# Performance work log

Hardware: AMD Instinct MI355X
Metric: run time of the kernel (lower is better)

## Reference

```python
import jax, jax.numpy as jnp
import numpy as np

SLOPE = 0.2

def setup_inputs() -> dict:
    key = jax.random.key(0)
    ks = jax.random.split(key, 24)
    B, O, M, Nb = 16, 1024, 64, 64
    in_ope, in_mas, in_arc, out = 16, 8, 8, 32
    f = lambda k, s: jax.random.normal(k, s, dtype=jnp.float32)
    adj = lambda k, s: jax.random.randint(k, s, 0, 2).astype(jnp.float32)
    return {
        'adj0': adj(ks[0], (O, M)),
        'adj1': adj(ks[1], (O, M)),
        'adj2': adj(ks[2], (O, Nb)),
        'adj3': adj(ks[3], (O, Nb)),
        'batch_idxes': jnp.arange(B, dtype=jnp.int64),
        'feat_opes': f(ks[4], (B, O, in_ope)),
        'feat_mas': f(ks[5], (B, M, in_mas)),
        'feat_buf': f(ks[6], (B, Nb, in_mas)),
        'feat_arc_ma_in': f(ks[7], (B, O, M, in_arc)),
        'feat_arc_buf_in': f(ks[8], (B, O, Nb, in_arc)),
        'feat_arc_ma_out': f(ks[9], (B, O, M, in_arc)),
        'feat_arc_buf_out': f(ks[10], (B, O, Nb, in_arc)),
        'W_ope': f(ks[11], (in_ope, out)) * 0.2,
        'W_mas': f(ks[12], (in_mas, out)) * 0.2,
        'W_buf': f(ks[13], (in_mas, out)) * 0.2,
        'W_arc_in': f(ks[14], (in_arc, out)) * 0.2,
        'W_arc_out': f(ks[15], (in_arc, out)) * 0.2,
        'attn_ope': jax.random.uniform(ks[16], (out,), dtype=jnp.float32),
        'attn_mas': jax.random.uniform(ks[17], (out,), dtype=jnp.float32),
        'attn_arc': jax.random.uniform(ks[18], (out,), dtype=jnp.float32),
    }

def _branch(adj_in, adj_out, p_ope, p_node, p_arc_in, p_arc_out, e_ope, e_node, e_arc_in, e_arc_out):
    # adj_*: [O,N]; e_ope: [B,O,1]; e_node: [B,N,1]; e_arc_*: [B,O,N,1]
    def scores(A2, e_arc):
        A = A2[None, :, :, None]                               # [1,O,N,1]
        a = A * e_ope[:, :, None, :] + e_arc + A * e_node[:, None, :, :]
        return jax.nn.leaky_relu(a, SLOPE)                     # [B,O,N,1]
    eik_in = scores(adj_in, e_arc_in)
    eik_out = scores(adj_out, e_arc_out)
    ekk = jax.nn.leaky_relu(e_node + e_node, SLOPE)            # [B,N,1]
    def alphas(A2, eik):
        e = jnp.concatenate([eik, ekk[:, None]], axis=1)       # [B,O+1,N,1]
        mask = jnp.concatenate([A2 == 1.0, jnp.ones((1, A2.shape[1]), dtype=bool)], axis=0)
        e = jnp.where(mask[None, :, :, None], e, -jnp.inf)
        return jax.nn.softmax(e[..., 0], axis=1)               # [B,O+1,N] over neighbors
    al_in = alphas(adj_in, eik_in)
    al_out = alphas(adj_out, eik_out)
    # NOTE: Wmu_out replicates the original's missing-parens expression exactly
    Wmu_in = jnp.sum((p_arc_in + p_ope[:, :, None, :]) * al_in[:, :-1, :, None], axis=1)   # [B,N,F]
    Wmu_out = jnp.sum(p_arc_out + p_ope[:, :, None, :] * al_out[:, :-1, :, None], axis=1)  # [B,N,F]
    Wmu_kk = p_node * (al_in[:, -1, :] + al_out[:, -1, :])[..., None]                      # [B,N,F]
    return jax.nn.sigmoid(Wmu_in + Wmu_out + Wmu_kk)

def reference(adj0, adj1, adj2, adj3, batch_idxes, feat_opes, feat_mas, feat_buf,
              feat_arc_ma_in, feat_arc_buf_in, feat_arc_ma_out, feat_arc_buf_out,
              W_ope, W_mas, W_buf, W_arc_in, W_arc_out, attn_ope, attn_mas, attn_arc):
    p_ope = feat_opes @ W_ope              # [B,O,F]
    p_mas = feat_mas @ W_mas               # [B,M,F]
    p_buf = feat_buf @ W_buf               # [B,Nb,F]
    p_arc_ma_in = feat_arc_ma_in @ W_arc_in
    p_arc_buf_in = feat_arc_buf_in @ W_arc_in
    p_arc_ma_out = feat_arc_ma_out @ W_arc_out
    p_arc_buf_out = feat_arc_buf_out @ W_arc_out
    score = lambda p, a: jnp.sum(p * a, axis=-1, keepdims=True)
    e_ope = score(p_ope, attn_ope)
    e_mas = score(p_mas, attn_mas)
    e_buf = score(p_buf, attn_mas)         # original uses attn_mas for buffers too
    nu_mas = _branch(adj0, adj1, p_ope, p_mas, p_arc_ma_in, p_arc_ma_out,
                     e_ope, e_mas, score(p_arc_ma_in, attn_arc), score(p_arc_ma_out, attn_arc))
    nu_buf = _branch(adj2, adj3, p_ope, p_buf, p_arc_buf_in, p_arc_buf_out,
                     e_ope, e_buf, score(p_arc_buf_in, attn_arc), score(p_arc_buf_out, attn_arc))
    return (nu_mas, nu_buf)
```

## Files before the change

### kernel.cpp

```cpp
#include <hip/hip_runtime.h>
#include <math.h>

#define B_   16
#define O_   1024
#define M_   64
#define C_   32
#define INO  16
#define INA  8
#define SLOPE 0.2f

#define NF    50
#define NCOL  (2*B_*M_)

#define WS_EOPE   0
#define WS_ENODE  (WS_EOPE + B_*O_)
#define WS_PNODE  (WS_ENODE + 2*B_*M_)
#define WS_WARC   (WS_PNODE + 2*B_*M_*C_)
#define WS_ACC    (WS_WARC + 16)

__device__ inline float rfl(float x) {
    return __int_as_float(__builtin_amdgcn_readfirstlane(__float_as_int(x)));
}

__global__ void k_pre(const float* __restrict__ feat_opes,
                      const float* __restrict__ feat_mas,
                      const float* __restrict__ feat_buf,
                      const float* __restrict__ W_ope,
                      const float* __restrict__ W_mas,
                      const float* __restrict__ W_buf,
                      const float* __restrict__ W_arc_in,
                      const float* __restrict__ W_arc_out,
                      const float* __restrict__ attn_ope,
                      const float* __restrict__ attn_mas,
                      const float* __restrict__ attn_arc,
                      float* __restrict__ ws) {
    int tid = threadIdx.x;
    int bid = blockIdx.x;
    if (bid < 64) {
        __shared__ float wo[INO];
        if (tid < INO) {
            float s = 0.f;
            for (int c = 0; c < C_; ++c) s += W_ope[tid*C_ + c]*attn_ope[c];
            wo[tid] = s;
        }
        __syncthreads();
        int idx = bid*256 + tid;
        const float* f = feat_opes + idx*INO;
        float s = 0.f;
#pragma unroll
        for (int j = 0; j < INO; ++j) s += f[j]*wo[j];
        ws[WS_EOPE + idx] = s;
    } else if (bid < 72) {
        int idx = (bid - 64)*256 + tid;
        int br  = idx >> 10;
        int rem = idx & 1023;
        const float* f = (br == 0 ? feat_mas : feat_buf) + rem*INA;
        const float* W = (br == 0 ? W_mas : W_buf);
        float f8[INA];
#pragma unroll
        for (int k = 0; k < INA; ++k) f8[k] = f[k];
        float e = 0.f;
        float* pn = ws + WS_PNODE + idx*C_;
        for (int c = 0; c < C_; ++c) {
            float s = 0.f;
#pragma unroll
            for (int k = 0; k < INA; ++k) s += f8[k]*W[k*C_ + c];
            pn[c] = s;
            e += s*attn_mas[c];
        }
        ws[WS_ENODE + idx] = e;
    } else if (bid == 72) {
        if (tid < 16) {
            const float* W = (tid < 8) ? W_arc_in : W_arc_out;
            int k = tid & 7;
            float s = 0.f;
            for (int c = 0; c < C_; ++c) s += W[k*C_ + c]*attn_arc[c];
            ws[WS_WARC + tid] = s;
        }
    } else {
        int idx = (bid - 73)*256 + tid;
        ws[WS_ACC + idx] = 0.f;
    }
}

__global__ __launch_bounds__(256) void k_main(
        const float* __restrict__ adj0, const float* __restrict__ adj1,
        const float* __restrict__ adj2, const float* __restrict__ adj3,
        const float* __restrict__ feat_opes,
        const float* __restrict__ fin_ma,  const float* __restrict__ fin_buf,
        const float* __restrict__ fout_ma, const float* __restrict__ fout_buf,
        float* __restrict__ ws) {
    int tid = threadIdx.x;
    int l  = tid & 63;
    int y  = __builtin_amdgcn_readfirstlane(tid >> 6);
    int oh = y & 1;
    int mh = y >> 1;
    int h  = l & 1;
    int m  = mh*32 + (l >> 1);
    int bid = blockIdx.x;
    int chunk = bid & 31;
    int t = bid >> 5;
    int b  = t & (B_ - 1);
    int br = t >> 4;
    int o0 = chunk*32 + oh*16;

    const float* A_in  = br ? adj2 : adj0;
    const float* A_out = br ? adj3 : adj1;
    const float* fin   = br ? fin_buf  : fin_ma;
    const float* fout  = br ? fout_buf : fout_ma;

    float4 wsi = *(const float4*)(ws + WS_WARC + h*4);
    float4 wso = *(const float4*)(ws + WS_WARC + 8 + h*4);

    float e_node_m = ws[WS_ENODE + (br*B_ + b)*M_ + m];

    const float* eop = ws + WS_EOPE + b*O_ + o0;
    float eo[16];
#pragma unroll
    for (int i = 0; i < 16; ++i) eo[i] = rfl(eop[i]);

    const float* Ai = A_in  + o0*M_ + m;
    const float* Ao = A_out + o0*M_ + m;
    unsigned amA = 0, amB = 0;
#pragma unroll
    for (int i = 0; i < 16; ++i) {
        amA |= (Ai[i*M_] == 1.0f) ? (1u << i) : 0u;
        amB |= (Ao[i*M_] == 1.0f) ? (1u << i) : 0u;
    }

    const float* Pi = fin  + ((size_t)(b*O_ + o0)*M_ + m)*INA + h*4;
    const float* Po = fout + ((size_t)(b*O_ + o0)*M_ + m)*INA + h*4;
    const float* fo = feat_opes + (size_t)(b*O_ + o0)*INO + h*8;
    const int OSTR = M_*INA;

    float l_in = 0.f, l_out = 0.f;
    float ai4[4], so4[4], aoi8[8], aoo8[8];
#pragma unroll
    for (int k = 0; k < 4; ++k) { ai4[k] = 0.f; so4[k] = 0.f; }
#pragma unroll
    for (int j = 0; j < 8; ++j) { aoi8[j] = 0.f; aoo8[j] = 0.f; }

#pragma unroll
    for (int it = 0; it < 16; ++it) {
        float4 xi = *(const float4*)(Pi + (size_t)it*OSTR);
        float4 xo = *(const float4*)(Po + (size_t)it*OSTR);
        float4 f0 = *(const float4*)(fo + it*INO);
        float4 f1 = *(const float4*)(fo + it*INO + 4);
        float pi_ = xi.x*wsi.x + xi.y*wsi.y + xi.z*wsi.z + xi.w*wsi.w;
        float po_ = xo.x*wso.x + xo.y*wso.y + xo.z*wso.z + xo.w*wso.w;
        float din = pi_ + __shfl_xor(pi_, 1, 64);
        float dot = po_ + __shfl_xor(po_, 1, 64);
        float base = eo[it] + e_node_m;
        float si = base + din;  si = si > 0.f ? si : SLOPE*si;
        float so = base + dot;  so = so > 0.f ? so : SLOPE*so;
        float wi  = (amA & (1u << it)) ? __expf(si) : 0.f;
        float wo_ = (amB & (1u << it)) ? __expf(so) : 0.f;
        l_in += wi; l_out += wo_;
        ai4[0] += wi*xi.x; ai4[1] += wi*xi.y; ai4[2] += wi*xi.z; ai4[3] += wi*xi.w;
        so4[0] += xo.x;    so4[1] += xo.y;    so4[2] += xo.z;    so4[3] += xo.w;
        aoi8[0] += wi*f0.x;  aoi8[1] += wi*f0.y;  aoi8[2] += wi*f0.z;  aoi8[3] += wi*f0.w;
        aoi8[4] += wi*f1.x;  aoi8[5] += wi*f1.y;  aoi8[6] += wi*f1.z;  aoi8[7] += wi*f1.w;
        aoo8[0] += wo_*f0.x; aoo8[1] += wo_*f0.y; aoo8[2] += wo_*f0.z; aoo8[3] += wo_*f0.w;
        aoo8[4] += wo_*f1.x; aoo8[5] += wo_*f1.y; aoo8[6] += wo_*f1.z; aoo8[7] += wo_*f1.w;
    }

    __shared__ float red[2][NF][64];
    if (h == 0) {
        red[oh][0][m]  = l_in;
        red[oh][25][m] = l_out;
#pragma unroll
        for (int k = 0; k < 4; ++k) { red[oh][1+k][m]  = ai4[k]; red[oh][42+k][m] = so4[k]; }
#pragma unroll
        for (int j = 0; j < 8; ++j) { red[oh][9+j][m]  = aoi8[j]; red[oh][26+j][m] = aoo8[j]; }
    } else {
#pragma unroll
        for (int k = 0; k < 4; ++k) { red[oh][5+k][m]  = ai4[k]; red[oh][46+k][m] = so4[k]; }
#pragma unroll
        for (int j = 0; j < 8; ++j) { red[oh][17+j][m] = aoi8[j]; red[oh][34+j][m] = aoo8[j]; }
    }
    __syncthreads();

    float* acc = ws + WS_ACC;
    int colbase = (br*B_ + b)*M_;
    for (int i = tid; i < NF*64; i += 256) {
        int f  = i >> 6;
        int m2 = i & 63;
        unsafeAtomicAdd(acc + f*NCOL + colbase + m2, red[0][f][m2] + red[1][f][m2]);
    }
}

__global__ __launch_bounds__(64) void k_fin(
        const float* __restrict__ W_ope,
        const float* __restrict__ W_arc_in,
        const float* __restrict__ W_arc_out,
        const float* __restrict__ ws,
        float* __restrict__ out) {
    int m = threadIdx.x;
    int bid = blockIdx.x;
    int b  = bid & (B_ - 1);
    int br = bid >> 4;
    int col = (br*B_ + b)*M_ + m;

    __shared__ float sW[1024];
    for (int i = m; i < 512; i += 64) sW[i] = W_ope[i];
    for (int i = m; i < 256; i += 64) { sW[512 + i] = W_arc_in[i]; sW[768 + i] = W_arc_out[i]; }
    __syncthreads();

    const float* acc = ws + WS_ACC;
    float v[NF];
#pragma unroll
    for (int f = 0; f < NF; ++f) v[f] = acc[f*NCOL + col];

    const float* pn = ws + WS_PNODE + col*C_;
    float pc[C_];
#pragma unroll
    for (int q = 0; q < 8; ++q) {
        float4 p4 = *(const float4*)(pn + 4*q);
        pc[4*q] = p4.x; pc[4*q+1] = p4.y; pc[4*q+2] = p4.z; pc[4*q+3] = p4.w;
    }

    float en  = ws[WS_ENODE + col];
    float ekk = 2.f*en; ekk = ekk > 0.f ? ekk : SLOPE*ekk;
    float wkk = __expf(ekk);

    float inv_i = 1.f / (v[0]  + wkk);
    float inv_o = 1.f / (v[25] + wkk);
    float akk   = wkk*inv_i + wkk*inv_o;

    float* op = out + (size_t)col*C_;
#pragma unroll 4
    for (int c = 0; c < C_; ++c) {
        float s_ai = 0.f, s_oi = 0.f, s_ao = 0.f, s_oo = 0.f;
#pragma unroll
        for (int k = 0; k < 8; ++k) {
            s_ai += v[1+k] *sW[512 + k*C_ + c];
            s_ao += v[42+k]*sW[768 + k*C_ + c];
        }
#pragma unroll
        for (int j = 0; j < 16; ++j) {
            float wv = sW[j*C_ + c];
            s_oi += v[9+j] *wv;
            s_oo += v[26+j]*wv;
        }
        float x = (s_ai + s_oi)*inv_i + s_ao + s_oo*inv_o + pc[c]*akk;
        op[c] = 1.f/(1.f + __expf(-x));
    }
}

extern "C" void kernel_launch(void* const* d_in, const int* in_sizes, int n_in,
                              void* d_out, int out_size, void* d_ws, size_t ws_size,
                              hipStream_t stream) {
    const float* adj0 = (const float*)d_in[0];
    const float* adj1 = (const float*)d_in[1];
    const float* adj2 = (const float*)d_in[2];
    const float* adj3 = (const float*)d_in[3];
    const float* feat_opes       = (const float*)d_in[5];
    const float* feat_mas        = (const float*)d_in[6];
    const float* feat_buf        = (const float*)d_in[7];
    const float* feat_arc_ma_in  = (const float*)d_in[8];
    const float* feat_arc_buf_in = (const float*)d_in[9];
    const float* feat_arc_ma_out = (const float*)d_in[10];
    const float* feat_arc_buf_out= (const float*)d_in[11];
    const float* W_ope    = (const float*)d_in[12];
    const float* W_mas    = (const float*)d_in[13];
    const float* W_buf    = (const float*)d_in[14];
    const float* W_arc_in = (const float*)d_in[15];
    const float* W_arc_out= (const float*)d_in[16];
    const float* attn_ope = (const float*)d_in[17];
    const float* attn_mas = (const float*)d_in[18];
    const float* attn_arc = (const float*)d_in[19];

    float* ws  = (float*)d_ws;
    float* out = (float*)d_out;

    k_pre<<<473, 256, 0, stream>>>(feat_opes, feat_mas, feat_buf,
                                   W_ope, W_mas, W_buf, W_arc_in, W_arc_out,
                                   attn_ope, attn_mas, attn_arc, ws);

    k_main<<<2*B_*32, 256, 0, stream>>>(adj0, adj1, adj2, adj3, feat_opes,
                                        feat_arc_ma_in, feat_arc_buf_in,
                                        feat_arc_ma_out, feat_arc_buf_out, ws);

    k_fin<<<2*B_, 64, 0, stream>>>(W_ope, W_arc_in, W_arc_out, ws, out);
}
```

Before: 216.9 us.

## Stage arc features through LDS with async global_load_lds double buffering

The main kernel now streams the per-(o,m) arc feature tiles into shared memory with global_load_lds DMA and a double buffer, computing one tile while the next one loads. The o-row assignment is interleaved across waves to match the tile layout, and the reduction buffer reuses the staging buffers. The aim is to overlap the memory-bound arc feature loads with the score and exp computation, at the cost of 32KB of LDS per block (lower occupancy) and extra barriers.

Measured after the change: 219.5 us. About the same (+1.2%).

```diff
diff --git a/kernel.cpp b/kernel.cpp
--- a/kernel.cpp
+++ b/kernel.cpp
@@ -20,6 +20,13 @@
 
 __device__ inline float rfl(float x) {
     return __int_as_float(__builtin_amdgcn_readfirstlane(__float_as_int(x)));
+}
+
+__device__ __forceinline__ void dma16(const float* g, float* l) {
+    __builtin_amdgcn_global_load_lds(
+        (const __attribute__((address_space(1))) void*)g,
+        (__attribute__((address_space(3))) void*)l,
+        16, 0, 0);
 }
 
 __global__ void k_pre(const float* __restrict__ feat_opes,
@@ -90,6 +97,9 @@
         const float* __restrict__ fin_ma,  const float* __restrict__ fin_buf,
         const float* __restrict__ fout_ma, const float* __restrict__ fout_buf,
         float* __restrict__ ws) {
+    __shared__ float sA[4096];
+    __shared__ float sB[4096];
+
     int tid = threadIdx.x;
     int l  = tid & 63;
     int y  = __builtin_amdgcn_readfirstlane(tid >> 6);
@@ -99,10 +109,10 @@
     int m  = mh*32 + (l >> 1);
     int bid = blockIdx.x;
     int chunk = bid & 31;
-    int t = bid >> 5;
-    int b  = t & (B_ - 1);
-    int br = t >> 4;
-    int o0 = chunk*32 + oh*16;
+    int t_ = bid >> 5;
+    int b  = t_ & (B_ - 1);
+    int br = t_ >> 4;
+    int o0 = chunk*32;
 
     const float* A_in  = br ? adj2 : adj0;
     const float* A_out = br ? adj3 : adj1;
@@ -114,24 +124,24 @@
 
     float e_node_m = ws[WS_ENODE + (br*B_ + b)*M_ + m];
 
-    const float* eop = ws + WS_EOPE + b*O_ + o0;
+    const float* eop = ws + WS_EOPE + b*O_ + o0 + oh*2;
     float eo[16];
 #pragma unroll
-    for (int i = 0; i < 16; ++i) eo[i] = rfl(eop[i]);
-
-    const float* Ai = A_in  + o0*M_ + m;
-    const float* Ao = A_out + o0*M_ + m;
+    for (int i = 0; i < 16; ++i) eo[i] = rfl(eop[(i >> 1)*4 + (i & 1)]);
+
+    const float* Ai = A_in  + (o0 + oh*2)*M_ + m;
+    const float* Ao = A_out + (o0 + oh*2)*M_ + m;
     unsigned amA = 0, amB = 0;
 #pragma unroll
     for (int i = 0; i < 16; ++i) {
-        amA |= (Ai[i*M_] == 1.0f) ? (1u << i) : 0u;
-        amB |= (Ao[i*M_] == 1.0f) ? (1u << i) : 0u;
-    }
-
-    const float* Pi = fin  + ((size_t)(b*O_ + o0)*M_ + m)*INA + h*4;
-    const float* Po = fout + ((size_t)(b*O_ + o0)*M_ + m)*INA + h*4;
-    const float* fo = feat_opes + (size_t)(b*O_ + o0)*INO + h*8;
-    const int OSTR = M_*INA;
+        int off = ((i >> 1)*4 + (i & 1))*M_;
+        amA |= (Ai[off] == 1.0f) ? (1u << i) : 0u;
+        amB |= (Ao[off] == 1.0f) ? (1u << i) : 0u;
+    }
+
+    const float* gin  = fin  + (size_t)(b*O_ + o0)*M_*INA;
+    const float* gout = fout + (size_t)(b*O_ + o0)*M_*INA;
+    const float* fo_b = feat_opes + (size_t)(b*O_ + o0)*INO + h*8;
 
     float l_in = 0.f, l_out = 0.f;
     float ai4[4], so4[4], aoi8[8], aoo8[8];
@@ -140,43 +150,81 @@
 #pragma unroll
     for (int j = 0; j < 8; ++j) { aoi8[j] = 0.f; aoo8[j] = 0.f; }
 
-#pragma unroll
-    for (int it = 0; it < 16; ++it) {
-        float4 xi = *(const float4*)(Pi + (size_t)it*OSTR);
-        float4 xo = *(const float4*)(Po + (size_t)it*OSTR);
-        float4 f0 = *(const float4*)(fo + it*INO);
-        float4 f1 = *(const float4*)(fo + it*INO + 4);
-        float pi_ = xi.x*wsi.x + xi.y*wsi.y + xi.z*wsi.z + xi.w*wsi.w;
-        float po_ = xo.x*wso.x + xo.y*wso.y + xo.z*wso.z + xo.w*wso.w;
-        float din = pi_ + __shfl_xor(pi_, 1, 64);
-        float dot = po_ + __shfl_xor(po_, 1, 64);
-        float base = eo[it] + e_node_m;
-        float si = base + din;  si = si > 0.f ? si : SLOPE*si;
-        float so = base + dot;  so = so > 0.f ? so : SLOPE*so;
-        float wi  = (amA & (1u << it)) ? __expf(si) : 0.f;
-        float wo_ = (amB & (1u << it)) ? __expf(so) : 0.f;
-        l_in += wi; l_out += wo_;
-        ai4[0] += wi*xi.x; ai4[1] += wi*xi.y; ai4[2] += wi*xi.z; ai4[3] += wi*xi.w;
-        so4[0] += xo.x;    so4[1] += xo.y;    so4[2] += xo.z;    so4[3] += xo.w;
-        aoi8[0] += wi*f0.x;  aoi8[1] += wi*f0.y;  aoi8[2] += wi*f0.z;  aoi8[3] += wi*f0.w;
-        aoi8[4] += wi*f1.x;  aoi8[5] += wi*f1.y;  aoi8[6] += wi*f1.z;  aoi8[7] += wi*f1.w;
-        aoo8[0] += wo_*f0.x; aoo8[1] += wo_*f0.y; aoo8[2] += wo_*f0.z; aoo8[3] += wo_*f0.w;
-        aoo8[4] += wo_*f1.x; aoo8[5] += wo_*f1.y; aoo8[6] += wo_*f1.z; aoo8[7] += wo_*f1.w;
-    }
-
-    __shared__ float red[2][NF][64];
+#define DMA_TILE(t, S)                                                     \
+    {                                                                      \
+        const float* gi = gin  + (size_t)(t)*2048;                         \
+        const float* go = gout + (size_t)(t)*2048;                         \
+        _Pragma("unroll")                                                  \
+        for (int i = 0; i < 2; ++i) {                                      \
+            int cf = (i*256 + y*64)*4;                                     \
+            dma16(gi + cf + l*4, S + cf);                                  \
+            dma16(go + cf + l*4, S + 2048 + cf);                           \
+        }                                                                  \
+    }
+
+#define COMP_TILE(t, S)                                                    \
+    {                                                                      \
+        _Pragma("unroll")                                                  \
+        for (int j = 0; j < 2; ++j) {                                      \
+            int ol  = oh*2 + j;                                            \
+            int idx = (t)*2 + j;                                           \
+            int o   = o0 + (t)*4 + ol;                                     \
+            float4 xi = *(const float4*)(S + ol*512 + mh*256 + l*4);       \
+            float4 xo = *(const float4*)(S + 2048 + ol*512 + mh*256 + l*4);\
+            const float* fop = fo_b + (size_t)(o - o0)*INO;                \
+            float4 f0 = *(const float4*)(fop);                             \
+            float4 f1 = *(const float4*)(fop + 4);                         \
+            float pi_ = xi.x*wsi.x + xi.y*wsi.y + xi.z*wsi.z + xi.w*wsi.w; \
+            float po_ = xo.x*wso.x + xo.y*wso.y + xo.z*wso.z + xo.w*wso.w; \
+            float din = pi_ + __shfl_xor(pi_, 1, 64);                      \
+            float dut = po_ + __shfl_xor(po_, 1, 64);                      \
+            float base = eo[idx] + e_node_m;                               \
+            float si = base + din;  si = si > 0.f ? si : SLOPE*si;         \
+            float so = base + dut;  so = so > 0.f ? so : SLOPE*so;         \
+            float wi  = (amA & (1u << idx)) ? __expf(si) : 0.f;            \
+            float wo_ = (amB & (1u << idx)) ? __expf(so) : 0.f;            \
+            l_in += wi; l_out += wo_;                                      \
+            ai4[0] += wi*xi.x; ai4[1] += wi*xi.y;                          \
+            ai4[2] += wi*xi.z; ai4[3] += wi*xi.w;                          \
+            so4[0] += xo.x;    so4[1] += xo.y;                             \
+            so4[2] += xo.z;    so4[3] += xo.w;                             \
+            aoi8[0] += wi*f0.x;  aoi8[1] += wi*f0.y;                       \
+            aoi8[2] += wi*f0.z;  aoi8[3] += wi*f0.w;                       \
+            aoi8[4] += wi*f1.x;  aoi8[5] += wi*f1.y;                       \
+            aoi8[6] += wi*f1.z;  aoi8[7] += wi*f1.w;                       \
+            aoo8[0] += wo_*f0.x; aoo8[1] += wo_*f0.y;                      \
+            aoo8[2] += wo_*f0.z; aoo8[3] += wo_*f0.w;                      \
+            aoo8[4] += wo_*f1.x; aoo8[5] += wo_*f1.y;                      \
+            aoo8[6] += wo_*f1.z; aoo8[7] += wo_*f1.w;                      \
+        }                                                                  \
+    }
+
+    DMA_TILE(0, sA);
+    __syncthreads();
+#pragma unroll
+    for (int tt = 0; tt < 4; ++tt) {
+        int t0 = tt*2;
+        if (t0 + 1 < 8) DMA_TILE(t0 + 1, sB);
+        COMP_TILE(t0, sA);
+        __syncthreads();
+        if (t0 + 2 < 8) DMA_TILE(t0 + 2, sA);
+        COMP_TILE(t0 + 1, sB);
+        __syncthreads();
+    }
+
+    float* red = oh ? sB : sA;
     if (h == 0) {
-        red[oh][0][m]  = l_in;
-        red[oh][25][m] = l_out;
-#pragma unroll
-        for (int k = 0; k < 4; ++k) { red[oh][1+k][m]  = ai4[k]; red[oh][42+k][m] = so4[k]; }
-#pragma unroll
-        for (int j = 0; j < 8; ++j) { red[oh][9+j][m]  = aoi8[j]; red[oh][26+j][m] = aoo8[j]; }
+        red[0*64 + m]  = l_in;
+        red[25*64 + m] = l_out;
+#pragma unroll
+        for (int k = 0; k < 4; ++k) { red[(1+k)*64 + m]  = ai4[k]; red[(42+k)*64 + m] = so4[k]; }
+#pragma unroll
+        for (int j = 0; j < 8; ++j) { red[(9+j)*64 + m]  = aoi8[j]; red[(26+j)*64 + m] = aoo8[j]; }
     } else {
 #pragma unroll
-        for (int k = 0; k < 4; ++k) { red[oh][5+k][m]  = ai4[k]; red[oh][46+k][m] = so4[k]; }
-#pragma unroll
-        for (int j = 0; j < 8; ++j) { red[oh][17+j][m] = aoi8[j]; red[oh][34+j][m] = aoo8[j]; }
+        for (int k = 0; k < 4; ++k) { red[(5+k)*64 + m]  = ai4[k]; red[(46+k)*64 + m] = so4[k]; }
+#pragma unroll
+        for (int j = 0; j < 8; ++j) { red[(17+j)*64 + m] = aoi8[j]; red[(34+j)*64 + m] = aoo8[j]; }
     }
     __syncthreads();
 
@@ -185,8 +233,10 @@
     for (int i = tid; i < NF*64; i += 256) {
         int f  = i >> 6;
         int m2 = i & 63;
-        unsafeAtomicAdd(acc + f*NCOL + colbase + m2, red[0][f][m2] + red[1][f][m2]);
-    }
+        unsafeAtomicAdd(acc + f*NCOL + colbase + m2, sA[f*64 + m2] + sB[f*64 + m2]);
+    }
+#undef DMA_TILE
+#undef COMP_TILE
 }
 
 __global__ __launch_bounds__(64) void k_fin(
```
